# Kernel optimization log

Measured on AMD Instinct MI355X. Metric: run time of the kernel, lower is better.

## Reference

```python
import jax, jax.numpy as jnp
import numpy as np

CLIP_MIN = 0.0  # recurrent_clip_min resolved in build() when -1
CLIP_MAX = 1.0  # recurrent_clip_max default when timesteps unknown


def setup_inputs() -> dict:
    key = jax.random.key(0)
    k1, k2, k3 = jax.random.split(key, 3)
    B, T, D, U = 64, 512, 256, 512
    x = jax.random.normal(k1, (B, T, D), dtype=jnp.float32)
    h0 = jnp.zeros((B, U), dtype=jnp.float32)
    W = jax.random.normal(k2, (D, U), dtype=jnp.float32) * (1.0 / np.sqrt(D))
    u = jax.random.uniform(k3, (U,), dtype=jnp.float32)  # uniform in clip range
    b = jnp.zeros((U,), dtype=jnp.float32)
    return {"x": x, "h0": h0, "W": W, "u": u, "b": b}


def reference(x, h0, W, u, b):
    # IndRNN: h_t = relu(x_t @ W + h_{t-1} * u + b), u clipped to [0, 1]
    u_c = jnp.clip(u, CLIP_MIN, CLIP_MAX)
    # One-time input projection for all timesteps: [B,T,U]
    proj = jnp.einsum("btd,du->btu", x, W) + b
    proj_t = jnp.swapaxes(proj, 0, 1)  # [T,B,U] for scan over time

    def step(h, p_t):
        h_new = jax.nn.relu(p_t + h * u_c)
        return h_new, h_new

    _, hs = jax.lax.scan(step, h0, proj_t)  # hs: [T,B,U]
    return jnp.swapaxes(hs, 0, 1)  # [B,T,U]
```

## Files before the change

### kernel.cpp

```cpp
#include <hip/hip_runtime.h>


__device__ __forceinline__ unsigned short f2bf(float f) {
    unsigned int u = __float_as_uint(f);
    unsigned int r = (u + 0x7FFF + ((u >> 16) & 1)) >> 16;
    return (unsigned short)r;
}

typedef __bf16 bf16x8 __attribute__((ext_vector_type(8)));
typedef float f32x4 __attribute__((ext_vector_type(4)));

typedef const unsigned char __attribute__((address_space(1))) gc_t;
typedef unsigned char __attribute__((address_space(3))) lds_t;

__device__ __forceinline__ void gl_lds16(const void* g, void* l) {
    __builtin_amdgcn_global_load_lds((gc_t*)g, (lds_t*)l, 16, 0, 0);
}

__global__ __launch_bounds__(256) void conv_x(
    const float* __restrict__ x, unsigned short* __restrict__ xb, int n4)
{
    int i = blockIdx.x * blockDim.x + threadIdx.x;
    if (i >= n4) return;
    float4 v = *(const float4*)(x + (long)i * 4);
    ushort4 o;
    o.x = f2bf(v.x); o.y = f2bf(v.y); o.z = f2bf(v.z); o.w = f2bf(v.w);
    *(ushort4*)(xb + (long)i * 4) = o;
}

__global__ __launch_bounds__(256) void conv_wt(
    const float* __restrict__ W, unsigned short* __restrict__ Wt, int K, int N)
{
    int idx = blockIdx.x * blockDim.x + threadIdx.x;
    int kq = K >> 2;
    if (idx >= N * kq) return;
    int n = idx / kq;
    int k4 = (idx - n * kq) * 4;
    ushort4 o;
    o.x = f2bf(W[(long)(k4 + 0) * N + n]);
    o.y = f2bf(W[(long)(k4 + 1) * N + n]);
    o.z = f2bf(W[(long)(k4 + 2) * N + n]);
    o.w = f2bf(W[(long)(k4 + 3) * N + n]);
    *(ushort4*)(Wt + (long)n * K + k4) = o;
}

#define TC 64
#define GN 128

__global__ __launch_bounds__(256, 1) void indrnn_fused(
    const unsigned short* __restrict__ xb,
    const unsigned short* __restrict__ wt,
    const float* __restrict__ bias,
    const float* __restrict__ h0,
    const float* __restrict__ uvec,
    float* __restrict__ out,
    int B, int T, int U)
{
    __shared__ char X[2][TC * 512];

    const int tid  = threadIdx.x;
    const int lane = tid & 63;
    const int w    = tid >> 6;
    const int m    = lane & 15;
    const int quad = lane >> 4;
    const int b    = blockIdx.x;
    const int n0   = blockIdx.y * GN;
    const int tq   = (w >> 1) * 32;
    const int cq   = (w & 1) * 64;

    bf16x8 bfr[4][8];
#pragma unroll
    for (int j = 0; j < 4; ++j)
#pragma unroll
        for (int kt = 0; kt < 8; ++kt)
            bfr[j][kt] = *(const bf16x8*)(
                wt + (long)(n0 + cq + j * 16 + m) * 256 + kt * 32 + quad * 8);

    float bb[4];
#pragma unroll
    for (int j = 0; j < 4; ++j) bb[j] = bias[n0 + cq + j * 16 + m];

    float uc = 0.0f, h = 0.0f;
    if (tid < GN) {
        uc = fminf(fmaxf(uvec[n0 + tid], 0.0f), 1.0f);
        h  = h0[(long)b * U + n0 + tid];
    }

    const unsigned short* xrow = xb + (long)b * T * 256;

    {
        const int p = lane & 31, hh = lane >> 5;
#pragma unroll
        for (int i = 0; i < 8; ++i) {
            int blk = i * 4 + w;
            int row = blk * 2 + hh;
            int gp  = p ^ (row & 15);
            gl_lds16(xrow + (long)row * 256 + gp * 8, &X[0][blk * 1024]);
        }
    }

    const int nch = T / TC;
    for (int c = 0; c < nch; ++c) {
        char* Xc = X[c & 1];
        __syncthreads();

        f32x4 acc[2][4];
#pragma unroll
        for (int i = 0; i < 2; ++i)
#pragma unroll
            for (int j = 0; j < 4; ++j) acc[i][j] = (f32x4){0.f, 0.f, 0.f, 0.f};

#pragma unroll
        for (int kt = 0; kt < 8; ++kt) {
            const int off = (((kt * 4 + quad) ^ m) * 16);
            bf16x8 a0 = *(const bf16x8*)(Xc + (tq + m) * 512 + off);
            bf16x8 a1 = *(const bf16x8*)(Xc + (tq + 16 + m) * 512 + off);
#pragma unroll
            for (int j = 0; j < 4; ++j) {
                acc[0][j] = __builtin_amdgcn_mfma_f32_16x16x32_bf16(
                    a0, bfr[j][kt], acc[0][j], 0, 0, 0);
                acc[1][j] = __builtin_amdgcn_mfma_f32_16x16x32_bf16(
                    a1, bfr[j][kt], acc[1][j], 0, 0, 0);
            }
        }
        __syncthreads();

        float* pf = (float*)Xc;
#pragma unroll
        for (int i = 0; i < 2; ++i)
#pragma unroll
            for (int j = 0; j < 4; ++j)
#pragma unroll
                for (int r = 0; r < 4; ++r) {
                    int tl  = tq + i * 16 + quad * 4 + r;
                    int col = cq + j * 16 + m;
                    int cs  = col ^ (quad << 4);
                    pf[tl * GN + cs] = acc[i][j][r] + bb[j];
                }
        __syncthreads();

        if (tid >= 128) {
            if (c + 1 < nch) {
                char* Xn = X[(c + 1) & 1];
                const unsigned short* gb = xrow + (long)(c + 1) * TC * 256;
                const int p = lane & 31, hh = lane >> 5;
#pragma unroll
                for (int i = 0; i < 16; ++i) {
                    int blk = i * 2 + (w - 2);
                    int row = blk * 2 + hh;
                    int gp  = p ^ (row & 15);
                    gl_lds16(gb + (long)row * 256 + gp * 8, Xn + blk * 1024);
                }
            }
        } else {
            const float* pfr = (const float*)Xc;
            float* og = out + ((long)b * T + c * TC) * U + n0 + tid;
#pragma unroll 8
            for (int t = 0; t < TC; ++t) {
                float pv = pfr[t * GN + (tid ^ (((t >> 2) & 3) << 4))];
                h = fmaxf(fmaf(h, uc, pv), 0.0f);
                og[(long)t * U] = h;
            }
        }
    }
}

#define BM 128
#define BN 128
#define BK 8

__global__ __launch_bounds__(256) void indrnn_gemm_bias(
    const float* __restrict__ A, const float* __restrict__ Bm,
    const float* __restrict__ bias, float* __restrict__ C,
    int M, int N, int K)
{
    __shared__ float As[BK][BM];
    __shared__ float Bs[BK][BN];
    const int tid = threadIdx.x;
    const int row0 = blockIdx.x * BM, col0 = blockIdx.y * BN;
    const int tx = tid & 15, ty = tid >> 4;
    float acc[8][8];
#pragma unroll
    for (int i = 0; i < 8; ++i)
#pragma unroll
        for (int j = 0; j < 8; ++j) acc[i][j] = 0.0f;
    const int am = tid >> 1, ak = (tid & 1) * 4;
    const int bk = tid >> 5, bn = (tid & 31) * 4;
    const float* Aptr = A + (long)(row0 + am) * K + ak;
    const float* Bptr = Bm + (long)bk * N + col0 + bn;
    for (int kt = 0; kt < K; kt += BK) {
        float4 av = *(const float4*)(Aptr + kt);
        float4 bv = *(const float4*)(Bptr + (long)kt * N);
        As[ak + 0][am] = av.x; As[ak + 1][am] = av.y;
        As[ak + 2][am] = av.z; As[ak + 3][am] = av.w;
        *(float4*)&Bs[bk][bn] = bv;
        __syncthreads();
#pragma unroll
        for (int k = 0; k < BK; ++k) {
            float4 a0 = *(const float4*)&As[k][ty * 4];
            float4 a1 = *(const float4*)&As[k][64 + ty * 4];
            float4 b0 = *(const float4*)&Bs[k][tx * 4];
            float4 b1 = *(const float4*)&Bs[k][64 + tx * 4];
            float a[8] = {a0.x, a0.y, a0.z, a0.w, a1.x, a1.y, a1.z, a1.w};
            float bb2[8] = {b0.x, b0.y, b0.z, b0.w, b1.x, b1.y, b1.z, b1.w};
#pragma unroll
            for (int i = 0; i < 8; ++i)
#pragma unroll
                for (int j = 0; j < 8; ++j)
                    acc[i][j] = fmaf(a[i], bb2[j], acc[i][j]);
        }
        __syncthreads();
    }
    float bb[8];
#pragma unroll
    for (int j = 0; j < 4; ++j) {
        bb[j] = bias[col0 + tx * 4 + j];
        bb[j + 4] = bias[col0 + 64 + tx * 4 + j];
    }
#pragma unroll
    for (int i = 0; i < 8; ++i) {
        const int r = (i < 4) ? (ty * 4 + i) : (64 + ty * 4 + (i - 4));
        float* crow = C + (long)(row0 + r) * N + col0;
        float4 v0 = {acc[i][0] + bb[0], acc[i][1] + bb[1], acc[i][2] + bb[2], acc[i][3] + bb[3]};
        float4 v1 = {acc[i][4] + bb[4], acc[i][5] + bb[5], acc[i][6] + bb[6], acc[i][7] + bb[7]};
        *(float4*)(crow + tx * 4) = v0;
        *(float4*)(crow + 64 + tx * 4) = v1;
    }
}

#define SCAN_UNROLL 32

__global__ __launch_bounds__(256) void indrnn_scan(
    float* __restrict__ out, const float* __restrict__ h0,
    const float* __restrict__ u, int B, int T, int U)
{
    const int idx = blockIdx.x * blockDim.x + threadIdx.x;
    if (idx >= B * U) return;
    const int b = idx / U;
    const int un = idx - b * U;
    const float uc = fminf(fmaxf(u[un], 0.0f), 1.0f);
    float h = h0[(long)b * U + un];
    float* p = out + (long)b * T * U + un;
    for (int t = 0; t < T; t += SCAN_UNROLL) {
        float pv[SCAN_UNROLL];
#pragma unroll
        for (int i = 0; i < SCAN_UNROLL; ++i)
            pv[i] = p[(long)(t + i) * U];
#pragma unroll
        for (int i = 0; i < SCAN_UNROLL; ++i) {
            h = fmaxf(fmaf(h, uc, pv[i]), 0.0f);
            pv[i] = h;
        }
#pragma unroll
        for (int i = 0; i < SCAN_UNROLL; ++i)
            p[(long)(t + i) * U] = pv[i];
    }
}

extern "C" void kernel_launch(void* const* d_in, const int* in_sizes, int n_in,
                              void* d_out, int out_size, void* d_ws, size_t ws_size,
                              hipStream_t stream) {
    const float* x  = (const float*)d_in[0];
    const float* h0 = (const float*)d_in[1];
    const float* W  = (const float*)d_in[2];
    const float* u  = (const float*)d_in[3];
    const float* b  = (const float*)d_in[4];
    float* out = (float*)d_out;

    const int U = in_sizes[3];
    const int B = in_sizes[1] / U;
    const int D = in_sizes[2] / U;
    const int T = in_sizes[0] / (B * D);
    const int M = B * T;

    const size_t xb_bytes = (size_t)M * D * sizeof(unsigned short);
    const size_t wt_bytes = (size_t)U * D * sizeof(unsigned short);
    const bool fused_ok = (D == 256) && (U % GN == 0) && (T % TC == 0) &&
                          (ws_size >= xb_bytes + wt_bytes);

    if (fused_ok) {
        unsigned short* xb = (unsigned short*)d_ws;
        unsigned short* wt = (unsigned short*)((char*)d_ws + xb_bytes);

        const int n4 = (M * D) / 4;
        conv_x<<<(n4 + 255) / 256, 256, 0, stream>>>(x, xb, n4);
        const int nwt = U * (D / 4);
        conv_wt<<<(nwt + 255) / 256, 256, 0, stream>>>(W, wt, D, U);

        dim3 g(B, U / GN);
        indrnn_fused<<<g, 256, 0, stream>>>(xb, wt, b, h0, u, out, B, T, U);
    } else {
        dim3 ggrid(M / BM, U / BN);
        indrnn_gemm_bias<<<ggrid, 256, 0, stream>>>(x, W, b, out, M, U, D);
        const int nthreads = B * U;
        indrnn_scan<<<(nthreads + 255) / 256, 256, 0, stream>>>(out, h0, u, B, T, U);
    }
}
```

Baseline: 121.1 us.

## Fuse fp32-to-bf16 input conversion into the IndRNN kernel and drop conv_x pass

Removes the separate conv_x kernel and its bf16 workspace. The fused kernel now loads fp32 x directly, converts it to bf16 in registers and writes it to swizzled LDS. A separate LDS buffer holds the projection results, so one barrier between the MFMA phase and the write-back goes away. In exchange, x is read as fp32 (twice the bytes) by each of the U-column blocks, and the staging is now synchronous register loads instead of async global-to-LDS loads.

```diff
diff --git a/kernel.cpp b/kernel.cpp
--- a/kernel.cpp
+++ b/kernel.cpp
@@ -1,4 +1,5 @@
 #include <hip/hip_runtime.h>
+#include <hip/hip_bf16.h>
 
 
 __device__ __forceinline__ unsigned short f2bf(float f) {
@@ -9,24 +10,6 @@
 
 typedef __bf16 bf16x8 __attribute__((ext_vector_type(8)));
 typedef float f32x4 __attribute__((ext_vector_type(4)));
-
-typedef const unsigned char __attribute__((address_space(1))) gc_t;
-typedef unsigned char __attribute__((address_space(3))) lds_t;
-
-__device__ __forceinline__ void gl_lds16(const void* g, void* l) {
-    __builtin_amdgcn_global_load_lds((gc_t*)g, (lds_t*)l, 16, 0, 0);
-}
-
-__global__ __launch_bounds__(256) void conv_x(
-    const float* __restrict__ x, unsigned short* __restrict__ xb, int n4)
-{
-    int i = blockIdx.x * blockDim.x + threadIdx.x;
-    if (i >= n4) return;
-    float4 v = *(const float4*)(x + (long)i * 4);
-    ushort4 o;
-    o.x = f2bf(v.x); o.y = f2bf(v.y); o.z = f2bf(v.z); o.w = f2bf(v.w);
-    *(ushort4*)(xb + (long)i * 4) = o;
-}
 
 __global__ __launch_bounds__(256) void conv_wt(
     const float* __restrict__ W, unsigned short* __restrict__ Wt, int K, int N)
@@ -47,8 +30,25 @@
 #define TC 64
 #define GN 128
 
+__device__ __forceinline__ void stage2(const float* __restrict__ g,
+                                       char* lds, int row0, int lane)
+{
+    const int r = row0 + (lane >> 5);
+    const int q = lane & 31;
+    const float* gp = g + (long)r * 256 + q * 8;
+    float4 a  = *(const float4*)gp;
+    float4 bq = *(const float4*)(gp + 4);
+    union { __hip_bfloat162 h; unsigned u; } c0, c1, c2, c3;
+    c0.h = __float22bfloat162_rn(make_float2(a.x, a.y));
+    c1.h = __float22bfloat162_rn(make_float2(a.z, a.w));
+    c2.h = __float22bfloat162_rn(make_float2(bq.x, bq.y));
+    c3.h = __float22bfloat162_rn(make_float2(bq.z, bq.w));
+    uint4 wv = {c0.u, c1.u, c2.u, c3.u};
+    *(uint4*)(lds + (long)r * 512 + ((q ^ (r & 15)) << 4)) = wv;
+}
+
 __global__ __launch_bounds__(256, 1) void indrnn_fused(
-    const unsigned short* __restrict__ xb,
+    const float* __restrict__ x,
     const unsigned short* __restrict__ wt,
     const float* __restrict__ bias,
     const float* __restrict__ h0,
@@ -56,7 +56,8 @@
     float* __restrict__ out,
     int B, int T, int U)
 {
-    __shared__ char X[2][TC * 512];
+    __shared__ __align__(16) char  Xa[2][TC * 512];
+    __shared__ __align__(16) float P[TC * GN];
 
     const int tid  = threadIdx.x;
     const int lane = tid & 63;
@@ -86,22 +87,15 @@
         h  = h0[(long)b * U + n0 + tid];
     }
 
-    const unsigned short* xrow = xb + (long)b * T * 256;
-
-    {
-        const int p = lane & 31, hh = lane >> 5;
-#pragma unroll
-        for (int i = 0; i < 8; ++i) {
-            int blk = i * 4 + w;
-            int row = blk * 2 + hh;
-            int gp  = p ^ (row & 15);
-            gl_lds16(xrow + (long)row * 256 + gp * 8, &X[0][blk * 1024]);
-        }
-    }
+    const float* xrow = x + (long)b * T * 256;
+
+#pragma unroll
+    for (int p = 0; p < 8; ++p)
+        stage2(xrow, Xa[0], w * 16 + p * 2, lane);
 
     const int nch = T / TC;
     for (int c = 0; c < nch; ++c) {
-        char* Xc = X[c & 1];
+        char* Xc = Xa[c & 1];
         __syncthreads();
 
         f32x4 acc[2][4];
@@ -112,7 +106,7 @@
 
 #pragma unroll
         for (int kt = 0; kt < 8; ++kt) {
-            const int off = (((kt * 4 + quad) ^ m) * 16);
+            const int off = (((kt * 4 + quad) ^ m) << 4);
             bf16x8 a0 = *(const bf16x8*)(Xc + (tq + m) * 512 + off);
             bf16x8 a1 = *(const bf16x8*)(Xc + (tq + 16 + m) * 512 + off);
 #pragma unroll
@@ -123,41 +117,32 @@
                     a1, bfr[j][kt], acc[1][j], 0, 0, 0);
             }
         }
-        __syncthreads();
-
-        float* pf = (float*)Xc;
+
 #pragma unroll
         for (int i = 0; i < 2; ++i)
 #pragma unroll
             for (int j = 0; j < 4; ++j)
 #pragma unroll
                 for (int r = 0; r < 4; ++r) {
-                    int tl  = tq + i * 16 + quad * 4 + r;
-                    int col = cq + j * 16 + m;
-                    int cs  = col ^ (quad << 4);
-                    pf[tl * GN + cs] = acc[i][j][r] + bb[j];
+                    int tl = tq + i * 16 + quad * 4 + r;
+                    int cs = (cq + j * 16 + m) ^ (quad << 4);
+                    P[tl * GN + cs] = acc[i][j][r] + bb[j];
                 }
         __syncthreads();
 
         if (tid >= 128) {
             if (c + 1 < nch) {
-                char* Xn = X[(c + 1) & 1];
-                const unsigned short* gb = xrow + (long)(c + 1) * TC * 256;
-                const int p = lane & 31, hh = lane >> 5;
-#pragma unroll
-                for (int i = 0; i < 16; ++i) {
-                    int blk = i * 2 + (w - 2);
-                    int row = blk * 2 + hh;
-                    int gp  = p ^ (row & 15);
-                    gl_lds16(gb + (long)row * 256 + gp * 8, Xn + blk * 1024);
-                }
+                const float* gnext = xrow + (long)(c + 1) * TC * 256;
+                char* Xn = Xa[(c + 1) & 1];
+#pragma unroll
+                for (int p = 0; p < 16; ++p)
+                    stage2(gnext, Xn, (w - 2) * 32 + p * 2, lane);
             }
         } else {
-            const float* pfr = (const float*)Xc;
-            float* og = out + ((long)b * T + c * TC) * U + n0 + tid;
+            float* og = out + ((long)b * T + (long)c * TC) * U + n0 + tid;
 #pragma unroll 8
             for (int t = 0; t < TC; ++t) {
-                float pv = pfr[t * GN + (tid ^ (((t >> 2) & 3) << 4))];
+                float pv = P[t * GN + (tid ^ (((t >> 2) & 3) << 4))];
                 h = fmaxf(fmaf(h, uc, pv), 0.0f);
                 og[(long)t * U] = h;
             }
@@ -273,22 +258,17 @@
     const int T = in_sizes[0] / (B * D);
     const int M = B * T;
 
-    const size_t xb_bytes = (size_t)M * D * sizeof(unsigned short);
     const size_t wt_bytes = (size_t)U * D * sizeof(unsigned short);
     const bool fused_ok = (D == 256) && (U % GN == 0) && (T % TC == 0) &&
-                          (ws_size >= xb_bytes + wt_bytes);
+                          (ws_size >= wt_bytes);
 
     if (fused_ok) {
-        unsigned short* xb = (unsigned short*)d_ws;
-        unsigned short* wt = (unsigned short*)((char*)d_ws + xb_bytes);
-
-        const int n4 = (M * D) / 4;
-        conv_x<<<(n4 + 255) / 256, 256, 0, stream>>>(x, xb, n4);
+        unsigned short* wt = (unsigned short*)d_ws;
         const int nwt = U * (D / 4);
         conv_wt<<<(nwt + 255) / 256, 256, 0, stream>>>(W, wt, D, U);
 
         dim3 g(B, U / GN);
-        indrnn_fused<<<g, 256, 0, stream>>>(xb, wt, b, h0, u, out, B, T, U);
+        indrnn_fused<<<g, 256, 0, stream>>>(x, wt, b, h0, u, out, B, T, U);
     } else {
         dim3 ggrid(M / BM, U / BN);
         indrnn_gemm_bias<<<ggrid, 256, 0, stream>>>(x, W, b, out, M, U, D);
```

After: 162.4 us. +34.2%, slower.

## Halve column tile per block, separate P buffer, merge conversion kernels

Applied to the files above, without the earlier changes.

Merges the x and W bf16 conversion kernels into a single launch. The fused kernel's column tile drops from 128 to 64 units, so twice as many blocks run and two can be resident per CU. A dedicated LDS buffer for the projected values removes one barrier per chunk. The cost is that each block reloads the same x chunk twice as often, and only one wave now runs the serial scan.

```diff
diff --git a/kernel.cpp b/kernel.cpp
--- a/kernel.cpp
+++ b/kernel.cpp
@@ -17,21 +17,19 @@
     __builtin_amdgcn_global_load_lds((gc_t*)g, (lds_t*)l, 16, 0, 0);
 }
 
-__global__ __launch_bounds__(256) void conv_x(
-    const float* __restrict__ x, unsigned short* __restrict__ xb, int n4)
+__global__ __launch_bounds__(256) void conv_xw(
+    const float* __restrict__ x, unsigned short* __restrict__ xb, int nx4,
+    const float* __restrict__ W, unsigned short* __restrict__ Wt, int K, int N)
 {
     int i = blockIdx.x * blockDim.x + threadIdx.x;
-    if (i >= n4) return;
-    float4 v = *(const float4*)(x + (long)i * 4);
-    ushort4 o;
-    o.x = f2bf(v.x); o.y = f2bf(v.y); o.z = f2bf(v.z); o.w = f2bf(v.w);
-    *(ushort4*)(xb + (long)i * 4) = o;
-}
-
-__global__ __launch_bounds__(256) void conv_wt(
-    const float* __restrict__ W, unsigned short* __restrict__ Wt, int K, int N)
-{
-    int idx = blockIdx.x * blockDim.x + threadIdx.x;
+    if (i < nx4) {
+        float4 v = *(const float4*)(x + (long)i * 4);
+        ushort4 o;
+        o.x = f2bf(v.x); o.y = f2bf(v.y); o.z = f2bf(v.z); o.w = f2bf(v.w);
+        *(ushort4*)(xb + (long)i * 4) = o;
+        return;
+    }
+    int idx = i - nx4;
     int kq = K >> 2;
     if (idx >= N * kq) return;
     int n = idx / kq;
@@ -45,9 +43,9 @@
 }
 
 #define TC 64
-#define GN 128
-
-__global__ __launch_bounds__(256, 1) void indrnn_fused(
+#define GN 64
+
+__global__ __launch_bounds__(256, 2) void indrnn_fused(
     const unsigned short* __restrict__ xb,
     const unsigned short* __restrict__ wt,
     const float* __restrict__ bias,
@@ -56,7 +54,8 @@
     float* __restrict__ out,
     int B, int T, int U)
 {
-    __shared__ char X[2][TC * 512];
+    __shared__ __align__(16) char  Xa[2][TC * 512];
+    __shared__ __align__(16) float P[TC * GN];
 
     const int tid  = threadIdx.x;
     const int lane = tid & 63;
@@ -65,8 +64,7 @@
     const int quad = lane >> 4;
     const int b    = blockIdx.x;
     const int n0   = blockIdx.y * GN;
-    const int tq   = (w >> 1) * 32;
-    const int cq   = (w & 1) * 64;
+    const int tq   = w * 16;
 
     bf16x8 bfr[4][8];
 #pragma unroll
@@ -74,11 +72,11 @@
 #pragma unroll
         for (int kt = 0; kt < 8; ++kt)
             bfr[j][kt] = *(const bf16x8*)(
-                wt + (long)(n0 + cq + j * 16 + m) * 256 + kt * 32 + quad * 8);
+                wt + (long)(n0 + j * 16 + m) * 256 + kt * 32 + quad * 8);
 
     float bb[4];
 #pragma unroll
-    for (int j = 0; j < 4; ++j) bb[j] = bias[n0 + cq + j * 16 + m];
+    for (int j = 0; j < 4; ++j) bb[j] = bias[n0 + j * 16 + m];
 
     float uc = 0.0f, h = 0.0f;
     if (tid < GN) {
@@ -93,71 +91,59 @@
 #pragma unroll
         for (int i = 0; i < 8; ++i) {
             int blk = i * 4 + w;
-            int row = blk * 2 + hh;
-            int gp  = p ^ (row & 15);
-            gl_lds16(xrow + (long)row * 256 + gp * 8, &X[0][blk * 1024]);
+            int r   = 2 * blk + hh;
+            int gp  = p ^ (r & 15);
+            gl_lds16(xrow + (long)r * 256 + gp * 8, &Xa[0][blk * 1024]);
         }
     }
 
     const int nch = T / TC;
     for (int c = 0; c < nch; ++c) {
-        char* Xc = X[c & 1];
-        __syncthreads();
-
-        f32x4 acc[2][4];
-#pragma unroll
-        for (int i = 0; i < 2; ++i)
-#pragma unroll
-            for (int j = 0; j < 4; ++j) acc[i][j] = (f32x4){0.f, 0.f, 0.f, 0.f};
+        const char* Xc = Xa[c & 1];
+        __syncthreads();
+
+        f32x4 acc[4];
+#pragma unroll
+        for (int j = 0; j < 4; ++j) acc[j] = (f32x4){0.f, 0.f, 0.f, 0.f};
 
 #pragma unroll
         for (int kt = 0; kt < 8; ++kt) {
-            const int off = (((kt * 4 + quad) ^ m) * 16);
-            bf16x8 a0 = *(const bf16x8*)(Xc + (tq + m) * 512 + off);
-            bf16x8 a1 = *(const bf16x8*)(Xc + (tq + 16 + m) * 512 + off);
-#pragma unroll
-            for (int j = 0; j < 4; ++j) {
-                acc[0][j] = __builtin_amdgcn_mfma_f32_16x16x32_bf16(
-                    a0, bfr[j][kt], acc[0][j], 0, 0, 0);
-                acc[1][j] = __builtin_amdgcn_mfma_f32_16x16x32_bf16(
-                    a1, bfr[j][kt], acc[1][j], 0, 0, 0);
+            bf16x8 a = *(const bf16x8*)(
+                Xc + (tq + m) * 512 + (((kt * 4 + quad) ^ m) << 4));
+#pragma unroll
+            for (int j = 0; j < 4; ++j)
+                acc[j] = __builtin_amdgcn_mfma_f32_16x16x32_bf16(
+                    a, bfr[j][kt], acc[j], 0, 0, 0);
+        }
+
+#pragma unroll
+        for (int j = 0; j < 4; ++j)
+#pragma unroll
+            for (int r = 0; r < 4; ++r) {
+                int tl = tq + quad * 4 + r;
+                int cs = (j * 16 + m) ^ (quad << 4);
+                P[tl * GN + cs] = acc[j][r] + bb[j];
             }
-        }
-        __syncthreads();
-
-        float* pf = (float*)Xc;
-#pragma unroll
-        for (int i = 0; i < 2; ++i)
-#pragma unroll
-            for (int j = 0; j < 4; ++j)
-#pragma unroll
-                for (int r = 0; r < 4; ++r) {
-                    int tl  = tq + i * 16 + quad * 4 + r;
-                    int col = cq + j * 16 + m;
-                    int cs  = col ^ (quad << 4);
-                    pf[tl * GN + cs] = acc[i][j][r] + bb[j];
-                }
-        __syncthreads();
-
-        if (tid >= 128) {
+        __syncthreads();
+
+        if (w >= 2) {
             if (c + 1 < nch) {
-                char* Xn = X[(c + 1) & 1];
                 const unsigned short* gb = xrow + (long)(c + 1) * TC * 256;
+                char* Xn = Xa[(c + 1) & 1];
                 const int p = lane & 31, hh = lane >> 5;
 #pragma unroll
                 for (int i = 0; i < 16; ++i) {
                     int blk = i * 2 + (w - 2);
-                    int row = blk * 2 + hh;
-                    int gp  = p ^ (row & 15);
-                    gl_lds16(gb + (long)row * 256 + gp * 8, Xn + blk * 1024);
+                    int r   = 2 * blk + hh;
+                    int gp  = p ^ (r & 15);
+                    gl_lds16(gb + (long)r * 256 + gp * 8, Xn + blk * 1024);
                 }
             }
-        } else {
-            const float* pfr = (const float*)Xc;
-            float* og = out + ((long)b * T + c * TC) * U + n0 + tid;
-#pragma unroll 8
+        } else if (w == 0) {
+            float* og = out + ((long)b * T + (long)c * TC) * U + n0 + lane;
+#pragma unroll 16
             for (int t = 0; t < TC; ++t) {
-                float pv = pfr[t * GN + (tid ^ (((t >> 2) & 3) << 4))];
+                float pv = P[t * GN + (lane ^ (((t >> 2) & 3) << 4))];
                 h = fmaxf(fmaf(h, uc, pv), 0.0f);
                 og[(long)t * U] = h;
             }
@@ -282,10 +268,10 @@
         unsigned short* xb = (unsigned short*)d_ws;
         unsigned short* wt = (unsigned short*)((char*)d_ws + xb_bytes);
 
-        const int n4 = (M * D) / 4;
-        conv_x<<<(n4 + 255) / 256, 256, 0, stream>>>(x, xb, n4);
+        const int nx4 = (M * D) / 4;
         const int nwt = U * (D / 4);
-        conv_wt<<<(nwt + 255) / 256, 256, 0, stream>>>(W, wt, D, U);
+        const int ntot = nx4 + nwt;
+        conv_xw<<<(ntot + 255) / 256, 256, 0, stream>>>(x, xb, nx4, W, wt, D, U);
 
         dim3 g(B, U / GN);
         indrnn_fused<<<g, 256, 0, stream>>>(xb, wt, b, h0, u, out, B, T, U);
```

New measurement: 127.8 us. 1.06x slower.
